# Kernel optimization log

Hardware: AMD Instinct MI355X
Metric: run time of the kernel (lower is better)

Reference implementation:

```python
import jax, jax.numpy as jnp
import numpy as np

N_ENTITIES = 100000
EMBED_DIM = 128
N_EDGES = 1600000
LEAKY_SLOPE = 0.01  # nn.LeakyReLU default


def setup_inputs() -> dict:
    key = jax.random.key(0)
    k1, k2, k3, k4, k5, k6, k7, k8 = jax.random.split(key, 8)
    entity_embs = jax.random.normal(k1, (N_ENTITIES, EMBED_DIM), dtype=jnp.float32)
    adj_rows = jax.random.randint(k2, (N_EDGES,), 0, N_ENTITIES, dtype=jnp.int32)
    adj_cols = jax.random.randint(k3, (N_EDGES,), 0, N_ENTITIES, dtype=jnp.int32)
    adj_vals = jax.random.uniform(k4, (N_EDGES,), dtype=jnp.float32)
    s = 1.0 / np.sqrt(EMBED_DIM)  # nn.Linear default init scale
    W_self = jax.random.uniform(k5, (EMBED_DIM, EMBED_DIM), jnp.float32, -s, s)
    b_self = jax.random.uniform(k6, (EMBED_DIM,), jnp.float32, -s, s)
    W_neigh = jax.random.uniform(k7, (EMBED_DIM, EMBED_DIM), jnp.float32, -s, s)
    b_neigh = jax.random.uniform(k8, (EMBED_DIM,), jnp.float32, -s, s)
    return {"entity_embs": entity_embs, "adj_rows": adj_rows, "adj_cols": adj_cols,
            "adj_vals": adj_vals, "W_self": W_self, "b_self": b_self,
            "W_neigh": W_neigh, "b_neigh": b_neigh}


def reference(entity_embs, adj_rows, adj_cols, adj_vals, W_self, b_self, W_neigh, b_neigh):
    # self path: Linear(input_dim, output_dim) -> x @ W.T + b
    self_emb = entity_embs @ W_self.T + b_self  # [N, D]
    # neighbor path: sparse adjacency SpMM (COO): out[r] += v * embs[c]
    contrib = adj_vals[:, None] * entity_embs[adj_cols]  # [E, D]
    neigh = jax.ops.segment_sum(contrib, adj_rows, num_segments=N_ENTITIES)  # [N, D]
    neigh_emb = neigh @ W_neigh.T + b_neigh
    out = jax.nn.leaky_relu(self_emb + neigh_emb, negative_slope=LEAKY_SLOPE)
    # dropout is identity in eval mode
    return out
```

## Files before the change

### kernel.cpp

```cpp
#include <hip/hip_runtime.h>

#define DIM 128
#define TILE_R 32
#define CAP 64
#define NREG 8
#define NCHUNK 128

typedef __attribute__((ext_vector_type(8))) short short8;
typedef __attribute__((ext_vector_type(4))) float floatx4;

static __device__ __forceinline__ short f2bf(float x) {
    unsigned u = __float_as_uint(x);
    u = (u + 0x7FFF + ((u >> 16) & 1)) >> 16;
    return (short)u;
}
static __device__ __forceinline__ float bflo(unsigned p) { return __uint_as_float(p << 16); }
static __device__ __forceinline__ float bfhi(unsigned p) { return __uint_as_float(p & 0xFFFF0000u); }

static __device__ __forceinline__ unsigned packcv(int c, float v) {
    int q = (int)(v * 32768.f + 0.5f);
    q = q > 32767 ? 32767 : q;
    return ((unsigned)c << 15) | (unsigned)q;
}

__global__ __launch_bounds__(256) void zero_kernel(float4* __restrict__ out, int n4) {
    int i = blockIdx.x * 256 + threadIdx.x;
    if (i < n4) out[i] = make_float4(0.f, 0.f, 0.f, 0.f);
}

__global__ __launch_bounds__(256) void zero_counts_kernel(int* __restrict__ cnt,
                                                          int* __restrict__ cursor, int n) {
    int i = blockIdx.x * 256 + threadIdx.x;
    if (i < n) cnt[i] = 0;
    if (i == 0) *cursor = 0;
}

__global__ __launch_bounds__(256) void prep_kernel(const float* __restrict__ Wself,
                                                   const float* __restrict__ Wneigh,
                                                   short* __restrict__ Wf,
                                                   int* __restrict__ next, int nRows) {
    int idx = blockIdx.x * 256 + threadIdx.x;
    if (idx < 4096) {
        int t = idx >> 8;
        int s = (idx >> 6) & 3;
        int lane = idx & 63;
        int n = (t & 7) * 16 + (lane & 15);
        int k0 = s * 32 + (lane >> 4) * 8;
        const float* row = (t < 8 ? Wself : Wneigh) + (size_t)n * DIM + k0;
        short8 v;
#pragma unroll
        for (int j = 0; j < 8; j++) v[j] = f2bf(row[j]);
        *(short8*)(Wf + (size_t)idx * 8) = v;
    }
    int r = idx - 4096;
    if (r >= 0 && r < nRows) next[r] = r * CAP;
}

__global__ __launch_bounds__(256) void pack_kernel(const int* __restrict__ cols,
                                                   const float* __restrict__ vals,
                                                   unsigned* __restrict__ pe, int nE) {
    int i4 = (blockIdx.x * 256 + threadIdx.x) * 4;
    if (i4 + 3 < nE) {
        int4 c = *(const int4*)(cols + i4);
        float4 v = *(const float4*)(vals + i4);
        uint4 o;
        o.x = packcv(c.x, v.x);
        o.y = packcv(c.y, v.y);
        o.z = packcv(c.z, v.z);
        o.w = packcv(c.w, v.w);
        *(uint4*)(pe + i4) = o;
    } else {
        for (int k = 0; k < 4 && i4 + k < nE; k++) pe[i4 + k] = packcv(cols[i4 + k], vals[i4 + k]);
    }
}

__global__ __launch_bounds__(256) void fill_xcd_pk_kernel(const int* __restrict__ rows,
                                                          const unsigned* __restrict__ pe,
                                                          int* __restrict__ next,
                                                          unsigned* __restrict__ pk,
                                                          int nE, int nRows) {
    int region = blockIdx.x & (NREG - 1);
    int chunk = blockIdx.x / NREG;
    int rowsPerReg = (nRows + NREG - 1) / NREG;
    int rowLo = region * rowsPerReg;
    int rowHi = min(rowLo + rowsPerReg, nRows);
    int per = (nE + NCHUNK - 1) / NCHUNK;
    per = (per + 3) & ~3;
    int s = chunk * per;
    int e = min(s + per, nE);

    for (int base = s + threadIdx.x * 4; base < e; base += 256 * 4) {
        int r4[4];
        unsigned p4[4];
        int cnt = 4;
        if (base + 3 < e) {
            int4 rv = *(const int4*)(rows + base);
            uint4 pv = *(const uint4*)(pe + base);
            r4[0] = rv.x; r4[1] = rv.y; r4[2] = rv.z; r4[3] = rv.w;
            p4[0] = pv.x; p4[1] = pv.y; p4[2] = pv.z; p4[3] = pv.w;
        } else {
            cnt = e - base;
            for (int k = 0; k < cnt; k++) {
                r4[k] = rows[base + k];
                p4[k] = pe[base + k];
            }
        }
#pragma unroll 4
        for (int k = 0; k < cnt; k++) {
            int rr = r4[k];
            if (rr >= rowLo && rr < rowHi) {
                int p = atomicAdd(&next[rr], 1);
                if (p < rr * CAP + CAP) pk[p] = p4[k];
            }
        }
    }
}

__global__ __launch_bounds__(256) void hist_kernel(const int* __restrict__ rows,
                                                   int* __restrict__ cnt, int nE) {
    int i4 = (blockIdx.x * 256 + threadIdx.x) * 4;
    if (i4 + 3 < nE) {
        int4 r = *(const int4*)(rows + i4);
        atomicAdd(&cnt[r.x], 1);
        atomicAdd(&cnt[r.y], 1);
        atomicAdd(&cnt[r.z], 1);
        atomicAdd(&cnt[r.w], 1);
    } else {
        for (int k = 0; k < 4 && i4 + k < nE; k++) atomicAdd(&cnt[rows[i4 + k]], 1);
    }
}

__global__ __launch_bounds__(256) void offsets_kernel(int* __restrict__ next,
                                                      int* __restrict__ start,
                                                      int* __restrict__ cursor, int n) {
    int i = blockIdx.x * 256 + threadIdx.x;
    int lane = threadIdx.x & 63;
    int c = (i < n) ? next[i] : 0;
    int s = c;
#pragma unroll
    for (int d = 1; d < 64; d <<= 1) {
        int t = __shfl_up(s, d);
        if (lane >= d) s += t;
    }
    int total = __shfl(s, 63);
    int base = 0;
    if (lane == 63) base = atomicAdd(cursor, total);
    base = __shfl(base, 63);
    int off = base + s - c;
    if (i < n) {
        start[i] = off;
        next[i] = off;
    }
}

__global__ __launch_bounds__(256) void fillB_kernel(const int* __restrict__ rows,
                                                    const int* __restrict__ cols,
                                                    const float* __restrict__ vals,
                                                    int* __restrict__ next,
                                                    int2* __restrict__ csr, int nE) {
    int i4 = (blockIdx.x * 256 + threadIdx.x) * 4;
    if (i4 + 3 < nE) {
        int4 r = *(const int4*)(rows + i4);
        int4 c = *(const int4*)(cols + i4);
        float4 v = *(const float4*)(vals + i4);
        int p0 = atomicAdd(&next[r.x], 1);
        int p1 = atomicAdd(&next[r.y], 1);
        int p2 = atomicAdd(&next[r.z], 1);
        int p3 = atomicAdd(&next[r.w], 1);
        csr[p0] = make_int2(c.x, __float_as_int(v.x));
        csr[p1] = make_int2(c.y, __float_as_int(v.y));
        csr[p2] = make_int2(c.z, __float_as_int(v.z));
        csr[p3] = make_int2(c.w, __float_as_int(v.w));
    } else {
        for (int k = 0; k < 4 && i4 + k < nE; k++) {
            int p = atomicAdd(&next[rows[i4 + k]], 1);
            csr[p] = make_int2(cols[i4 + k], __float_as_int(vals[i4 + k]));
        }
    }
}

__global__ __launch_bounds__(256) void wprep_kernel(const float* __restrict__ Wself,
                                                    const float* __restrict__ Wneigh,
                                                    short* __restrict__ Wf) {
    int idx = blockIdx.x * 256 + threadIdx.x;
    int t = idx >> 8;
    int s = (idx >> 6) & 3;
    int lane = idx & 63;
    int n = (t & 7) * 16 + (lane & 15);
    int k0 = s * 32 + (lane >> 4) * 8;
    const float* row = (t < 8 ? Wself : Wneigh) + (size_t)n * DIM + k0;
    short8 v;
#pragma unroll
    for (int j = 0; j < 8; j++) v[j] = f2bf(row[j]);
    *(short8*)(Wf + (size_t)idx * 8) = v;
}

__global__ __launch_bounds__(256) void gemm4_kernel(const float* __restrict__ embs,
                                                    const short* __restrict__ Wf,
                                                    unsigned short* __restrict__ Sb,
                                                    unsigned short* __restrict__ Yb,
                                                    int nRows) {
    int wave = threadIdx.x >> 6;
    int lane = threadIdx.x & 63;
    int quad = lane >> 4;
    int m0 = blockIdx.x * 256 + wave * 64;

    short8 a[4][4];
#pragma unroll
    for (int rt = 0; rt < 4; rt++) {
        int m = m0 + rt * 16 + (lane & 15);
        bool valid = m < nRows;
        const float* Arow = embs + (size_t)m * DIM;
#pragma unroll
        for (int s = 0; s < 4; s++) {
            float4 f0 = make_float4(0.f, 0.f, 0.f, 0.f), f1 = f0;
            if (valid) {
                f0 = *(const float4*)(Arow + s * 32 + quad * 8);
                f1 = *(const float4*)(Arow + s * 32 + quad * 8 + 4);
            }
            short8 av;
            av[0] = f2bf(f0.x); av[1] = f2bf(f0.y); av[2] = f2bf(f0.z); av[3] = f2bf(f0.w);
            av[4] = f2bf(f1.x); av[5] = f2bf(f1.y); av[6] = f2bf(f1.z); av[7] = f2bf(f1.w);
            a[rt][s] = av;
        }
    }

    const short8* WfV = (const short8*)Wf;
#pragma unroll
    for (int t = 0; t < 16; t++) {
        floatx4 acc0 = {0.f, 0.f, 0.f, 0.f};
        floatx4 acc1 = acc0, acc2 = acc0, acc3 = acc0;
#pragma unroll
        for (int s = 0; s < 4; s++) {
            short8 b = WfV[(t * 4 + s) * 64 + lane];
            acc0 = __builtin_amdgcn_mfma_f32_16x16x32_bf16(a[0][s], b, acc0, 0, 0, 0);
            acc1 = __builtin_amdgcn_mfma_f32_16x16x32_bf16(a[1][s], b, acc1, 0, 0, 0);
            acc2 = __builtin_amdgcn_mfma_f32_16x16x32_bf16(a[2][s], b, acc2, 0, 0, 0);
            acc3 = __builtin_amdgcn_mfma_f32_16x16x32_bf16(a[3][s], b, acc3, 0, 0, 0);
        }
        int col = t * 16 + (lane & 15);
        unsigned short* dst = (col < DIM) ? (Sb + col) : (Yb + (col - DIM));
#pragma unroll
        for (int reg = 0; reg < 4; reg++) {
            int g0 = m0 + quad * 4 + reg;
            int g1 = g0 + 16, g2 = g0 + 32, g3 = g0 + 48;
            if (g0 < nRows) dst[(size_t)g0 * DIM] = (unsigned short)f2bf(acc0[reg]);
            if (g1 < nRows) dst[(size_t)g1 * DIM] = (unsigned short)f2bf(acc1[reg]);
            if (g2 < nRows) dst[(size_t)g2 * DIM] = (unsigned short)f2bf(acc2[reg]);
            if (g3 < nRows) dst[(size_t)g3 * DIM] = (unsigned short)f2bf(acc3[reg]);
        }
    }
}

__global__ __launch_bounds__(256) void gatherY_pk_kernel(const unsigned* __restrict__ Sb,
                                                         const unsigned* __restrict__ Yb,
                                                         const int* __restrict__ rowEnd,
                                                         const unsigned* __restrict__ pk,
                                                         const float* __restrict__ bself,
                                                         const float* __restrict__ bneigh,
                                                         float* __restrict__ out, int nRows) {
    int r = blockIdx.x * 4 + (threadIdx.x >> 6);
    if (r >= nRows) return;
    int lane = threadIdx.x & 63;
    int s = r * CAP;
    int e = min(__builtin_amdgcn_readfirstlane(rowEnd[r]), s + CAP);
    float ax = 0.f, ay = 0.f;
    const float qs = 1.f / 32768.f;
    int j = s;
    for (; j + 4 <= e; j += 4) {
        uint4 q = *(const uint4*)(pk + j);
        unsigned y0 = Yb[(size_t)(q.x >> 15) * 64 + lane];
        unsigned y1 = Yb[(size_t)(q.y >> 15) * 64 + lane];
        unsigned y2 = Yb[(size_t)(q.z >> 15) * 64 + lane];
        unsigned y3 = Yb[(size_t)(q.w >> 15) * 64 + lane];
        float v0 = (float)(q.x & 32767u) * qs;
        float v1 = (float)(q.y & 32767u) * qs;
        float v2 = (float)(q.z & 32767u) * qs;
        float v3 = (float)(q.w & 32767u) * qs;
        ax += v0 * bflo(y0) + v1 * bflo(y1) + v2 * bflo(y2) + v3 * bflo(y3);
        ay += v0 * bfhi(y0) + v1 * bfhi(y1) + v2 * bfhi(y2) + v3 * bfhi(y3);
    }
    for (; j < e; j++) {
        unsigned q = pk[j];
        float v = (float)(q & 32767u) * qs;
        unsigned y = Yb[(size_t)(q >> 15) * 64 + lane];
        ax += v * bflo(y);
        ay += v * bfhi(y);
    }
    unsigned sp = __builtin_nontemporal_load(&Sb[(size_t)r * 64 + lane]);
    float ox = bflo(sp) + bself[2 * lane] + bneigh[2 * lane] + ax;
    float oy = bfhi(sp) + bself[2 * lane + 1] + bneigh[2 * lane + 1] + ay;
    ox = ox > 0.f ? ox : 0.01f * ox;
    oy = oy > 0.f ? oy : 0.01f * oy;
    union { float2 f; double d; } u;
    u.f = make_float2(ox, oy);
    __builtin_nontemporal_store(u.d, (double*)(out + (size_t)r * DIM + lane * 2));
}

__global__ __launch_bounds__(256) void gatherY_kernel(const unsigned* __restrict__ Sb,
                                                      const unsigned* __restrict__ Yb,
                                                      const int* __restrict__ start,
                                                      const int* __restrict__ next,
                                                      const int2* __restrict__ csr,
                                                      const float* __restrict__ bself,
                                                      const float* __restrict__ bneigh,
                                                      float* __restrict__ out, int nRows) {
    int r = blockIdx.x * 4 + (threadIdx.x >> 6);
    if (r >= nRows) return;
    int lane = threadIdx.x & 63;
    int s = __builtin_amdgcn_readfirstlane(start[r]);
    int e = __builtin_amdgcn_readfirstlane(next[r]);
    float ax = 0.f, ay = 0.f;
    int j = s;
    for (; j + 4 <= e; j += 4) {
        int2 c0 = csr[j], c1 = csr[j + 1], c2 = csr[j + 2], c3 = csr[j + 3];
        unsigned y0 = Yb[(size_t)c0.x * 64 + lane];
        unsigned y1 = Yb[(size_t)c1.x * 64 + lane];
        unsigned y2 = Yb[(size_t)c2.x * 64 + lane];
        unsigned y3 = Yb[(size_t)c3.x * 64 + lane];
        float v0 = __int_as_float(c0.y), v1 = __int_as_float(c1.y);
        float v2 = __int_as_float(c2.y), v3 = __int_as_float(c3.y);
        ax += v0 * bflo(y0) + v1 * bflo(y1) + v2 * bflo(y2) + v3 * bflo(y3);
        ay += v0 * bfhi(y0) + v1 * bfhi(y1) + v2 * bfhi(y2) + v3 * bfhi(y3);
    }
    for (; j < e; j++) {
        int2 c = csr[j];
        float v = __int_as_float(c.y);
        unsigned y = Yb[(size_t)c.x * 64 + lane];
        ax += v * bflo(y);
        ay += v * bfhi(y);
    }
    unsigned sp = __builtin_nontemporal_load(&Sb[(size_t)r * 64 + lane]);
    float ox = bflo(sp) + bself[2 * lane] + bneigh[2 * lane] + ax;
    float oy = bfhi(sp) + bself[2 * lane + 1] + bneigh[2 * lane + 1] + ay;
    ox = ox > 0.f ? ox : 0.01f * ox;
    oy = oy > 0.f ? oy : 0.01f * oy;
    union { float2 f; double d; } u;
    u.f = make_float2(ox, oy);
    __builtin_nontemporal_store(u.d, (double*)(out + (size_t)r * DIM + lane * 2));
}

__global__ __launch_bounds__(256) void gather_embs_kernel(const float2* __restrict__ embs2,
                                                          const int* __restrict__ start,
                                                          const int* __restrict__ next,
                                                          const int2* __restrict__ csr,
                                                          float* __restrict__ out, int nRows) {
    int r = blockIdx.x * 4 + (threadIdx.x >> 6);
    if (r >= nRows) return;
    int lane = threadIdx.x & 63;
    int s = start[r];
    int e = next[r];
    float2 acc = make_float2(0.f, 0.f);
    for (int b = s; b < e; b += 64) {
        int n = min(64, e - b);
        int2 cv = make_int2(0, 0);
        if (lane < n) cv = csr[b + lane];
        float vf = __int_as_float(cv.y);
        for (int j = 0; j < n; j++) {
            int cj = __shfl(cv.x, j);
            float vj = __shfl(vf, j);
            float2 x = embs2[(size_t)cj * 64 + lane];
            acc.x += vj * x.x;
            acc.y += vj * x.y;
        }
    }
    ((float2*)out)[(size_t)r * 64 + lane] = acc;
}

__global__ __launch_bounds__(256) void scatter_kernel(
    const float* __restrict__ embs, const int* __restrict__ rows,
    const int* __restrict__ cols, const float* __restrict__ vals,
    float* __restrict__ out, int nE) {
    int e = blockIdx.x * 4 + (threadIdx.x >> 6);
    if (e >= nE) return;
    int lane = threadIdx.x & 63;
    int r = rows[e];
    int c = cols[e];
    float v = vals[e];
    float2 x = ((const float2*)(embs + (size_t)c * DIM))[lane];
    float* dst = out + (size_t)r * DIM + lane * 2;
    unsafeAtomicAdd(dst, v * x.x);
    unsafeAtomicAdd(dst + 1, v * x.y);
}

__global__ __launch_bounds__(256) void fused_kernel(
    const float* __restrict__ embs, const float* __restrict__ Wself,
    const float* __restrict__ bself, const float* __restrict__ Wneigh,
    const float* __restrict__ bneigh, float* __restrict__ out, int nRows) {
    __shared__ float xs[TILE_R][DIM];
    __shared__ float xn[TILE_R][DIM];

    int r0 = blockIdx.x * TILE_R;
    if (r0 >= nRows) return;

    const float4* gs = (const float4*)(embs + (size_t)r0 * DIM);
    const float4* gn = (const float4*)(out + (size_t)r0 * DIM);
    float4* sxs = (float4*)&xs[0][0];
    float4* sxn = (float4*)&xn[0][0];
    for (int i = threadIdx.x; i < TILE_R * DIM / 4; i += 256) {
        sxs[i] = gs[i];
        sxn[i] = gn[i];
    }
    __syncthreads();

    int j = threadIdx.x & 127;
    int rbase = (threadIdx.x >> 7) * 16;

    const float4* ws = (const float4*)(Wself + (size_t)j * DIM);
    const float4* wn = (const float4*)(Wneigh + (size_t)j * DIM);

    float acc[16];
#pragma unroll
    for (int i = 0; i < 16; i++) acc[i] = 0.f;

    for (int k4 = 0; k4 < DIM / 4; k4++) {
        float4 a = ws[k4];
        float4 b = wn[k4];
#pragma unroll
        for (int rr = 0; rr < 16; rr++) {
            float4 x = *(const float4*)&xs[rbase + rr][k4 * 4];
            float4 y = *(const float4*)&xn[rbase + rr][k4 * 4];
            acc[rr] += x.x * a.x + x.y * a.y + x.z * a.z + x.w * a.w
                     + y.x * b.x + y.y * b.y + y.z * b.z + y.w * b.w;
        }
    }

    float bias = bself[j] + bneigh[j];
#pragma unroll
    for (int rr = 0; rr < 16; rr++) {
        float v = acc[rr] + bias;
        out[(size_t)(r0 + rbase + rr) * DIM + j] = v > 0.f ? v : 0.01f * v;
    }
}

static inline size_t a16(size_t x) { return (x + 15) & ~(size_t)15; }

extern "C" void kernel_launch(void* const* d_in, const int* in_sizes, int n_in,
                              void* d_out, int out_size, void* d_ws, size_t ws_size,
                              hipStream_t stream) {
    const float* embs   = (const float*)d_in[0];
    const int*   rows   = (const int*)d_in[1];
    const int*   cols   = (const int*)d_in[2];
    const float* vals   = (const float*)d_in[3];
    const float* Wself  = (const float*)d_in[4];
    const float* bself  = (const float*)d_in[5];
    const float* Wneigh = (const float*)d_in[6];
    const float* bneigh = (const float*)d_in[7];
    float* out = (float*)d_out;

    int nE = in_sizes[1];
    int nRows = out_size / DIM;
    size_t wfBytes = (size_t)16 * 4 * 64 * 8 * 2;
    size_t bfPlane = (size_t)nRows * DIM * 2;

    size_t A7_next = 0;
    size_t A7_buck = A7_next + a16((size_t)nRows * 4);
    size_t A7_pe   = A7_buck + a16((size_t)nRows * CAP * 4);
    size_t A7_wf   = A7_pe + a16((size_t)nE * 4);
    size_t A7_y    = A7_wf + a16(wfBytes);
    size_t A7_s    = A7_y + bfPlane;
    size_t needA7  = A7_s + bfPlane;
    bool   okA7    = nRows <= (1 << 17);

    size_t B_next  = 0;
    size_t B_start = B_next + a16((size_t)nRows * 4);
    size_t B_cur   = B_start + a16((size_t)nRows * 4);
    size_t B_csr   = B_cur + 16;
    size_t B_wf    = B_csr + a16((size_t)nE * 8);
    size_t B_y     = B_wf + a16(wfBytes);
    size_t B_s     = B_y + bfPlane;
    size_t needB   = B_s + bfPlane;

    size_t C_csr  = a16((size_t)(2 * nRows + 1) * 4);
    size_t needC  = C_csr + (size_t)nE * 8;

    int rb = (nRows + 255) / 256;
    int eb4 = (nE / 4 + 255) / 256;
    int ebp = ((nE + 3) / 4 + 255) / 256;

    if (okA7 && ws_size >= needA7) {
        int*      next = (int*)((char*)d_ws + A7_next);
        unsigned* pk   = (unsigned*)((char*)d_ws + A7_buck);
        unsigned* pe   = (unsigned*)((char*)d_ws + A7_pe);
        short*    Wf   = (short*)((char*)d_ws + A7_wf);
        unsigned short* Yb = (unsigned short*)((char*)d_ws + A7_y);
        unsigned short* Sb = (unsigned short*)((char*)d_ws + A7_s);

        prep_kernel<<<(4096 + nRows + 255) / 256, 256, 0, stream>>>(Wself, Wneigh, Wf, next, nRows);
        pack_kernel<<<ebp, 256, 0, stream>>>(cols, vals, pe, nE);
        fill_xcd_pk_kernel<<<NREG * NCHUNK, 256, 0, stream>>>(rows, pe, next, pk, nE, nRows);
        gemm4_kernel<<<(nRows + 255) / 256, 256, 0, stream>>>(embs, Wf, Sb, Yb, nRows);
        gatherY_pk_kernel<<<(nRows + 3) / 4, 256, 0, stream>>>(
            (const unsigned*)Sb, (const unsigned*)Yb, next, pk, bself, bneigh, out, nRows);
    } else if (ws_size >= needB) {
        int*  next   = (int*)((char*)d_ws + B_next);
        int*  start  = (int*)((char*)d_ws + B_start);
        int*  cursor = (int*)((char*)d_ws + B_cur);
        int2* csr    = (int2*)((char*)d_ws + B_csr);
        short* Wf    = (short*)((char*)d_ws + B_wf);
        unsigned short* Yb = (unsigned short*)((char*)d_ws + B_y);
        unsigned short* Sb = (unsigned short*)((char*)d_ws + B_s);

        zero_counts_kernel<<<rb, 256, 0, stream>>>(next, cursor, nRows);
        hist_kernel<<<eb4, 256, 0, stream>>>(rows, next, nE);
        offsets_kernel<<<rb, 256, 0, stream>>>(next, start, cursor, nRows);
        fillB_kernel<<<eb4, 256, 0, stream>>>(rows, cols, vals, next, csr, nE);
        wprep_kernel<<<16, 256, 0, stream>>>(Wself, Wneigh, Wf);
        gemm4_kernel<<<(nRows + 255) / 256, 256, 0, stream>>>(embs, Wf, Sb, Yb, nRows);
        gatherY_kernel<<<(nRows + 3) / 4, 256, 0, stream>>>(
            (const unsigned*)Sb, (const unsigned*)Yb, start, next, csr,
            bself, bneigh, out, nRows);
    } else if (ws_size >= needC) {
        int* next = (int*)d_ws;
        int* start = next + nRows;
        int* cursor = start + nRows;
        int2* csr = (int2*)((char*)d_ws + C_csr);

        zero_counts_kernel<<<rb, 256, 0, stream>>>(next, cursor, nRows);
        hist_kernel<<<eb4, 256, 0, stream>>>(rows, next, nE);
        offsets_kernel<<<rb, 256, 0, stream>>>(next, start, cursor, nRows);
        fillB_kernel<<<eb4, 256, 0, stream>>>(rows, cols, vals, next, csr, nE);
        gather_embs_kernel<<<(nRows + 3) / 4, 256, 0, stream>>>(
            (const float2*)embs, start, next, csr, out, nRows);
        fused_kernel<<<(nRows + TILE_R - 1) / TILE_R, 256, 0, stream>>>(
            embs, Wself, bself, Wneigh, bneigh, out, nRows);
    } else {
        int n4 = out_size / 4;
        zero_kernel<<<(n4 + 255) / 256, 256, 0, stream>>>((float4*)out, n4);
        scatter_kernel<<<(nE + 3) / 4, 256, 0, stream>>>(embs, rows, cols, vals, out, nE);
        fused_kernel<<<(nRows + TILE_R - 1) / TILE_R, 256, 0, stream>>>(
            embs, Wself, bself, Wneigh, bneigh, out, nRows);
    }
}
```

Before: 297.8 us.

## Pre-split edges into per-region queues before bucket fill

Adds a new default path. A split kernel packs col/val per edge, determines which of the 8 row regions the edge belongs to, and appends it to a per-region queue using block-local counts plus one global atomic per region per block. A fill2 kernel then maps blocks to regions (blockIdx & 7), with each region's queue divided into 96 chunks, and scatters the queued entries into the fixed-capacity row buckets. This replaces the separate pack pass and the region-filtered fill pass, aiming to avoid repeated scans of the edge arrays and to keep each region's bucket atomics on one XCD. In exchange it adds an extra int2 queue write and read, and a fixed queue capacity that silently drops edges if a region overflows it. The fallback A7 path now passes the next array as qcount, so its first entries get zeroed.

```diff
diff --git a/kernel.cpp b/kernel.cpp
--- a/kernel.cpp
+++ b/kernel.cpp
@@ -5,6 +5,7 @@
 #define CAP 64
 #define NREG 8
 #define NCHUNK 128
+#define NCH2 96
 
 typedef __attribute__((ext_vector_type(8))) short short8;
 typedef __attribute__((ext_vector_type(4))) float floatx4;
@@ -21,6 +22,13 @@
     int q = (int)(v * 32768.f + 0.5f);
     q = q > 32767 ? 32767 : q;
     return ((unsigned)c << 15) | (unsigned)q;
+}
+
+static __device__ __forceinline__ int regionOf(int rr, int rpr) {
+    int reg = (rr >= (rpr << 2)) ? 4 : 0;
+    reg += (rr >= (reg + 2) * rpr) ? 2 : 0;
+    reg += (rr >= (reg + 1) * rpr) ? 1 : 0;
+    return reg;
 }
 
 __global__ __launch_bounds__(256) void zero_kernel(float4* __restrict__ out, int n4) {
@@ -38,7 +46,8 @@
 __global__ __launch_bounds__(256) void prep_kernel(const float* __restrict__ Wself,
                                                    const float* __restrict__ Wneigh,
                                                    short* __restrict__ Wf,
-                                                   int* __restrict__ next, int nRows) {
+                                                   int* __restrict__ next,
+                                                   int* __restrict__ qcount, int nRows) {
     int idx = blockIdx.x * 256 + threadIdx.x;
     if (idx < 4096) {
         int t = idx >> 8;
@@ -54,6 +63,82 @@
     }
     int r = idx - 4096;
     if (r >= 0 && r < nRows) next[r] = r * CAP;
+    int z = idx - 4096 - nRows;
+    if (z >= 0 && z < NREG) qcount[z] = 0;
+}
+
+__global__ __launch_bounds__(256) void split_kernel(const int* __restrict__ rows,
+                                                    const int* __restrict__ cols,
+                                                    const float* __restrict__ vals,
+                                                    int2* __restrict__ rq,
+                                                    int* __restrict__ qcount,
+                                                    int nE, int nRows, int qcap) {
+    __shared__ int lcnt[NREG];
+    __shared__ int lbase[NREG];
+    __shared__ int lcur[NREG];
+    int rpr = (nRows + NREG - 1) / NREG;
+    int i4 = (blockIdx.x * 256 + threadIdx.x) * 4;
+
+    if (threadIdx.x < NREG) lcnt[threadIdx.x] = 0;
+    __syncthreads();
+
+    int r4[4];
+    unsigned p4[4];
+    int rg4[4];
+    int cnt = 0;
+    if (i4 + 3 < nE) {
+        int4 r = *(const int4*)(rows + i4);
+        int4 c = *(const int4*)(cols + i4);
+        float4 v = *(const float4*)(vals + i4);
+        r4[0] = r.x; r4[1] = r.y; r4[2] = r.z; r4[3] = r.w;
+        p4[0] = packcv(c.x, v.x); p4[1] = packcv(c.y, v.y);
+        p4[2] = packcv(c.z, v.z); p4[3] = packcv(c.w, v.w);
+        cnt = 4;
+    } else {
+        for (int k = 0; k < 4 && i4 + k < nE; k++) {
+            r4[cnt] = rows[i4 + k];
+            p4[cnt] = packcv(cols[i4 + k], vals[i4 + k]);
+            cnt++;
+        }
+    }
+#pragma unroll 4
+    for (int k = 0; k < cnt; k++) {
+        rg4[k] = regionOf(r4[k], rpr);
+        atomicAdd(&lcnt[rg4[k]], 1);
+    }
+    __syncthreads();
+    if (threadIdx.x < NREG) {
+        lbase[threadIdx.x] = atomicAdd(&qcount[threadIdx.x], lcnt[threadIdx.x]);
+        lcur[threadIdx.x] = 0;
+    }
+    __syncthreads();
+#pragma unroll 4
+    for (int k = 0; k < cnt; k++) {
+        int rg = rg4[k];
+        int pos = lbase[rg] + atomicAdd(&lcur[rg], 1);
+        if (pos < qcap) rq[(size_t)rg * qcap + pos] = make_int2(r4[k], (int)p4[k]);
+    }
+}
+
+__global__ __launch_bounds__(256) void fill2_kernel(const int2* __restrict__ rq,
+                                                    const int* __restrict__ qcount,
+                                                    int* __restrict__ next,
+                                                    unsigned* __restrict__ pk,
+                                                    int qcap) {
+    int region = blockIdx.x & (NREG - 1);
+    int chunk = blockIdx.x >> 3;
+    int n = qcount[region];
+    if (n > qcap) n = qcap;
+    int per = (n + NCH2 - 1) / NCH2;
+    int s = chunk * per;
+    int e = min(s + per, n);
+    const int2* q = rq + (size_t)region * qcap;
+    for (int i = s + threadIdx.x; i < e; i += 256) {
+        int2 ent = q[i];
+        int rr = ent.x;
+        int p = atomicAdd(&next[rr], 1);
+        if (p < rr * CAP + CAP) pk[p] = (unsigned)ent.y;
+    }
 }
 
 __global__ __launch_bounds__(256) void pack_kernel(const int* __restrict__ cols,
@@ -452,6 +537,17 @@
     int nRows = out_size / DIM;
     size_t wfBytes = (size_t)16 * 4 * 64 * 8 * 2;
     size_t bfPlane = (size_t)nRows * DIM * 2;
+    int qcap = nE / NREG + 8192;
+
+    size_t A8_next = 0;
+    size_t A8_qc   = A8_next + a16((size_t)nRows * 4);
+    size_t A8_buck = A8_qc + a16((size_t)NREG * 4);
+    size_t A8_rq   = A8_buck + a16((size_t)nRows * CAP * 4);
+    size_t A8_wf   = A8_rq + a16((size_t)NREG * qcap * 8);
+    size_t A8_y    = A8_wf + a16(wfBytes);
+    size_t A8_s    = A8_y + bfPlane;
+    size_t needA8  = A8_s + bfPlane;
+    bool   okA8    = nRows <= (1 << 17);
 
     size_t A7_next = 0;
     size_t A7_buck = A7_next + a16((size_t)nRows * 4);
@@ -478,7 +574,23 @@
     int eb4 = (nE / 4 + 255) / 256;
     int ebp = ((nE + 3) / 4 + 255) / 256;
 
-    if (okA7 && ws_size >= needA7) {
+    if (okA8 && ws_size >= needA8) {
+        int*      next   = (int*)((char*)d_ws + A8_next);
+        int*      qcount = (int*)((char*)d_ws + A8_qc);
+        unsigned* pk     = (unsigned*)((char*)d_ws + A8_buck);
+        int2*     rq     = (int2*)((char*)d_ws + A8_rq);
+        short*    Wf     = (short*)((char*)d_ws + A8_wf);
+        unsigned short* Yb = (unsigned short*)((char*)d_ws + A8_y);
+        unsigned short* Sb = (unsigned short*)((char*)d_ws + A8_s);
+
+        prep_kernel<<<(4096 + nRows + NREG + 255) / 256, 256, 0, stream>>>(
+            Wself, Wneigh, Wf, next, qcount, nRows);
+        split_kernel<<<ebp, 256, 0, stream>>>(rows, cols, vals, rq, qcount, nE, nRows, qcap);
+        fill2_kernel<<<NREG * NCH2, 256, 0, stream>>>(rq, qcount, next, pk, qcap);
+        gemm4_kernel<<<(nRows + 255) / 256, 256, 0, stream>>>(embs, Wf, Sb, Yb, nRows);
+        gatherY_pk_kernel<<<(nRows + 3) / 4, 256, 0, stream>>>(
+            (const unsigned*)Sb, (const unsigned*)Yb, next, pk, bself, bneigh, out, nRows);
+    } else if (okA7 && ws_size >= needA7) {
         int*      next = (int*)((char*)d_ws + A7_next);
         unsigned* pk   = (unsigned*)((char*)d_ws + A7_buck);
         unsigned* pe   = (unsigned*)((char*)d_ws + A7_pe);
@@ -486,7 +598,8 @@
         unsigned short* Yb = (unsigned short*)((char*)d_ws + A7_y);
         unsigned short* Sb = (unsigned short*)((char*)d_ws + A7_s);
 
-        prep_kernel<<<(4096 + nRows + 255) / 256, 256, 0, stream>>>(Wself, Wneigh, Wf, next, nRows);
+        prep_kernel<<<(4096 + nRows + NREG + 255) / 256, 256, 0, stream>>>(
+            Wself, Wneigh, Wf, next, (int*)((char*)d_ws + A7_next), nRows);
         pack_kernel<<<ebp, 256, 0, stream>>>(cols, vals, pe, nE);
         fill_xcd_pk_kernel<<<NREG * NCHUNK, 256, 0, stream>>>(rows, pe, next, pk, nE, nRows);
         gemm4_kernel<<<(nRows + 255) / 256, 256, 0, stream>>>(embs, Wf, Sb, Yb, nRows);
```

New measurement: 323.6 us. +8.7%, slower.
